# Optimization experiments

Measured on AMD Instinct MI355X. Metric: run time of the kernel, lower is better.

## Reference

```python
import jax, jax.numpy as jnp
import numpy as np

B, IN_DIM, OUT_DIM = 16384, 1024, 512
N_CAPS, CAP_DIM = 8, 16


def squash(x, axis=-1):
    # scale = |x|^2 / (1 + |x|^2) ; out = scale * x / sqrt(|x|^2 + 1e-8)
    sq = jnp.sum(x * x, axis=axis, keepdims=True)
    return (sq / (1.0 + sq)) * x / jnp.sqrt(sq + 1e-8)


def setup_inputs() -> dict:
    key = jax.random.key(0)
    k1, k2, k3, k4 = jax.random.split(key, 4)
    x = jax.random.normal(k1, (B, IN_DIM), dtype=jnp.float32)
    # Linear(in_dim, n_caps*cap_dim) params (kaiming-ish scale)
    Wp = jax.random.normal(k2, (IN_DIM, N_CAPS * CAP_DIM), dtype=jnp.float32) / np.sqrt(IN_DIM)
    bp = jax.random.normal(k3, (N_CAPS * CAP_DIM,), dtype=jnp.float32) * 0.01
    # routing transform W: [n_caps, cap_dim, out_dim], init std 0.02 as in torch code
    W = jax.random.normal(k4, (N_CAPS, CAP_DIM, OUT_DIM), dtype=jnp.float32) * 0.02
    return {"x": x, "Wp": Wp, "bp": bp, "W": W, "n_routing": 3}


def reference(x, Wp, bp, W, n_routing):
    batch = x.shape[0]
    primary = x @ Wp + bp                                   # [B, n*d]
    primary = primary.reshape(batch, N_CAPS, CAP_DIM)       # [B, n, d]
    primary = squash(primary, axis=-1)
    u_hat = jnp.einsum('bnd,ndo->bno', primary, W)          # [B, n, o]
    b = jnp.zeros((batch, N_CAPS, 1), dtype=x.dtype)
    v = None
    for i in range(n_routing):
        c = jax.nn.softmax(b, axis=1)                       # [B, n, 1]
        s = jnp.sum(c * u_hat, axis=1)                      # [B, o]
        v = squash(s, axis=-1)                              # [B, o]
        if i < n_routing - 1:
            agreement = jnp.einsum('bno,bo->bn', u_hat, v)  # [B, n]
            b = b + agreement[..., None]
    return v
```

## Files before the change

kernel.cpp:

```cpp
#include <hip/hip_runtime.h>
#include <hip/hip_bf16.h>
#include <math.h>

typedef __attribute__((ext_vector_type(8))) short bf16x8;
typedef __attribute__((ext_vector_type(8))) unsigned short u16x8;
typedef __attribute__((ext_vector_type(4))) float f32x4;
typedef __attribute__((ext_vector_type(16))) float f32x16;

__device__ __forceinline__ unsigned short f2bf(float f) {
  unsigned u = __float_as_uint(f);
  return (unsigned short)((u + 0x7FFFu + ((u >> 16) & 1u)) >> 16);
}
__device__ __forceinline__ float bf2f(unsigned short h) {
  return __uint_as_float(((unsigned)h) << 16);
}
__device__ __forceinline__ void cvt8pk(const float4& a, const float4& b,
                                       u16x8& h, u16x8& l) {
  float f[8] = {a.x, a.y, a.z, a.w, b.x, b.y, b.z, b.w};
  unsigned* hp = (unsigned*)&h;
  unsigned* lp = (unsigned*)&l;
#pragma unroll
  for (int i = 0; i < 4; ++i) {
    __hip_bfloat162 hb = __float22bfloat162_rn(make_float2(f[2*i], f[2*i+1]));
    unsigned hv = *(unsigned*)&hb;
    hp[i] = hv;
    float r0 = f[2*i]     - __uint_as_float(hv << 16);
    float r1 = f[2*i + 1] - __uint_as_float(hv & 0xFFFF0000u);
    __hip_bfloat162 lb = __float22bfloat162_rn(make_float2(r0, r1));
    lp[i] = *(unsigned*)&lb;
  }
}
__device__ __forceinline__ void cvt8b(const float4& a, const float4& b,
                                      bf16x8& h, bf16x8& l) {
  u16x8 hh, ll;
  cvt8pk(a, b, hh, ll);
  h = *(bf16x8*)&hh;
  l = *(bf16x8*)&ll;
}

#define GLD16(g, l) __builtin_amdgcn_global_load_lds( \
    (const __attribute__((address_space(1))) void*)(g), \
    (__attribute__((address_space(3))) void*)(l), 16, 0, 0)

#define MFMA32(a, b, c) __builtin_amdgcn_mfma_f32_32x32x16_bf16(a, b, c, 0, 0, 0)

__device__ const int PM36[36] = {0,0,0,0,0,0,0,0, 1,1,1,1,1,1,1, 2,2,2,2,2,2,
                                 3,3,3,3,3, 4,4,4,4, 5,5,5, 6,6, 7};
__device__ const int PN36[36] = {0,1,2,3,4,5,6,7, 1,2,3,4,5,6,7, 2,3,4,5,6,7,
                                 3,4,5,6,7, 4,5,6,7, 5,6,7, 6,7, 7};
__device__ __forceinline__ constexpr int gidx(int a, int b) {
  int m = a < b ? a : b, n = a < b ? b : a;
  return m * 8 - (m * (m - 1)) / 2 + (n - m);
}

__global__ __launch_bounds__(256) void caps_prep_all(
    const float* __restrict__ Wp, const float* __restrict__ W,
    unsigned short* __restrict__ th1, unsigned short* __restrict__ tl1,
    unsigned short* __restrict__ th2, unsigned short* __restrict__ tl2,
    float* __restrict__ M)
{
  __shared__ float tile[64][128];
  const int t = threadIdx.x, b = blockIdx.x;
  if (b < 16) {
    const float* src = Wp + (size_t)b * 64 * 128;
#pragma unroll
    for (int i = 0; i < 8; ++i) {
      int j = t + i * 256;
      int kk = j >> 5, q = j & 31;
      *(float4*)&tile[kk][q * 4] = *(const float4*)(src + kk * 128 + q * 4);
    }
    __syncthreads();
    const int col = t >> 1, kg0 = (t & 1) * 4;
    unsigned short hi[32], lo[32];
#pragma unroll
    for (int kk = 0; kk < 32; ++kk) {
      float v = tile[kg0 * 8 + kk][col];
      unsigned short h = f2bf(v);
      hi[kk] = h;
      lo[kk] = f2bf(v - bf2f(h));
    }
#pragma unroll
    for (int i = 0; i < 4; ++i) {
      size_t off = (size_t)b * 8192 + (size_t)(kg0 + i) * 1024 + (size_t)col * 8;
      u16x8 vh, vl;
#pragma unroll
      for (int e = 0; e < 8; ++e) { vh[e] = hi[i * 8 + e]; vl[e] = lo[i * 8 + e]; }
      *(u16x8*)(th1 + off) = vh;
      *(u16x8*)(tl1 + off) = vl;
    }
  } else if (b < 32) {
    int tt = (b - 16) * 256 + t;
#pragma unroll
    for (int h = 0; h < 2; ++h) {
      int c = tt + h * 4096;
      int kt = c >> 12, rem = c & 4095;
      int kg = rem >> 9, col = rem & 511;
      int kbase = kt * 64 + kg * 8;
      u16x8 vh, vl;
#pragma unroll
      for (int e = 0; e < 8; ++e) {
        float v = W[(size_t)(kbase + e) * 512 + col];
        unsigned short hh = f2bf(v);
        vh[e] = hh;
        vl[e] = f2bf(v - bf2f(hh));
      }
      size_t off = ((size_t)(kt * 8 + kg) * 512 + col) * 8;
      *(u16x8*)(th2 + off) = vh;
      *(u16x8*)(tl2 + off) = vl;
    }
  } else {
    int bb = b - 32;
    int a = (bb >> 3) * 16 + (t >> 4);
    int c = (bb & 7) * 16 + (t & 15);
    const float* wa = W + (size_t)a * 512;
    const float* wb = W + (size_t)c * 512;
    float acc = 0.f;
#pragma unroll 4
    for (int o = 0; o < 512; o += 4) {
      float4 xx = *(const float4*)(wa + o);
      float4 yy = *(const float4*)(wb + o);
      acc += xx.x * yy.x + xx.y * yy.y + xx.z * yy.z + xx.w * yy.w;
    }
    M[a * 128 + c] = acc;
  }
}

#define K1BUF 20480

__global__ __launch_bounds__(256) void caps_primary(
    const float* __restrict__ x, const unsigned short* __restrict__ bth,
    const unsigned short* __restrict__ btl, const float* __restrict__ bp,
    float* __restrict__ p_out)
{
  __shared__ unsigned short lds[2 * K1BUF];
  const int tid  = threadIdx.x;
  const int lane = tid & 63;
  const int wn   = tid >> 6;
  const int lc   = lane & 31;
  const int hi   = lane >> 5;
  const int row0 = blockIdx.x * 32;

  const int rowA = tid & 31;
  const int kgA  = tid >> 5;
  const float* xrow = x + (size_t)(row0 + rowA) * 1024 + kgA * 8;

  f32x16 acc;
#pragma unroll
  for (int j = 0; j < 16; ++j) acc[j] = 0.f;

  float4 a0, a1;

#define A_LOAD(kt) do { const float* xp_ = xrow + (kt) * 64; \
    a0 = *(const float4*)(xp_); a1 = *(const float4*)(xp_ + 4); } while (0)

#define B_ISSUE(kt, bufi) do { \
    unsigned short* Bh_ = lds + (bufi) * K1BUF + 4096; \
    unsigned short* Bl_ = lds + (bufi) * K1BUF + 12288; \
    const unsigned short* gh_ = bth + ((size_t)(kt) * 1024 + tid) * 8; \
    const unsigned short* gl_ = btl + ((size_t)(kt) * 1024 + tid) * 8; \
    _Pragma("unroll") for (int c_ = 0; c_ < 4; ++c_) { \
      GLD16(gh_ + c_ * 2048, Bh_ + (c_ * 256 + tid) * 8); \
      GLD16(gl_ + c_ * 2048, Bl_ + (c_ * 256 + tid) * 8); \
    } } while (0)

#define A_WRITE(bufi) do { u16x8 h_, l_; cvt8pk(a0, a1, h_, l_); \
    unsigned short* A_ = lds + (bufi) * K1BUF; \
    *(u16x8*)(A_ + (kgA * 32 + rowA) * 8) = h_; \
    *(u16x8*)(A_ + 2048 + (kgA * 32 + rowA) * 8) = l_; } while (0)

#define COMPUTE(bufi) do { \
    const unsigned short* F = lds + (bufi) * K1BUF; \
    _Pragma("unroll") \
    for (int kk = 0; kk < 4; ++kk) { \
      const int ks = kk * 2 + hi; \
      bf16x8 ah  = *(const bf16x8*)(F + (ks * 32 + lc) * 8); \
      bf16x8 al  = *(const bf16x8*)(F + 2048 + (ks * 32 + lc) * 8); \
      bf16x8 bh  = *(const bf16x8*)(F + 4096  + (ks * 128 + wn * 32 + lc) * 8); \
      bf16x8 blo = *(const bf16x8*)(F + 12288 + (ks * 128 + wn * 32 + lc) * 8); \
      acc = MFMA32(ah, bh,  acc); \
      acc = MFMA32(ah, blo, acc); \
      acc = MFMA32(al, bh,  acc); \
    } } while (0)

  A_LOAD(0);
  B_ISSUE(0, 0);
  A_WRITE(0);
  __syncthreads();

#pragma unroll 2
  for (int kt = 0; kt < 16; ++kt) {
    const int cur = kt & 1;
    if (kt < 15) {
      A_LOAD(kt + 1);
      B_ISSUE(kt + 1, cur ^ 1);
    }
    COMPUTE(cur);
    if (kt < 15) A_WRITE(cur ^ 1);
    __syncthreads();
  }
#undef A_LOAD
#undef B_ISSUE
#undef A_WRITE
#undef COMPUTE

  const int col = wn * 32 + lc;
  const float bpv = bp[col];
#pragma unroll
  for (int r = 0; r < 16; ++r) {
    const int row = (r & 3) + 8 * (r >> 2) + 4 * hi;
    float val = acc[r] + bpv;
    float sq = val * val;
    sq += __shfl_xor(sq, 1); sq += __shfl_xor(sq, 2);
    sq += __shfl_xor(sq, 4); sq += __shfl_xor(sq, 8);
    float sc = (sq / (1.f + sq)) / sqrtf(sq + 1e-8f);
    p_out[(size_t)(row0 + row) * 128 + col] = val * sc;
  }
}

__global__ __launch_bounds__(256, 1) void caps_route_g(
    const float* __restrict__ p_in, const float* __restrict__ Mg,
    float* __restrict__ qout)
{
  __shared__ float p_lds[128 * 66];
  __shared__ float M_lds[16384];
  __shared__ float G_lds[64 * 37];
  __shared__ float cs_lds[64 * 9];
  const int tid  = threadIdx.x;
  const int lane = tid & 63;
  const int w    = tid >> 6;
  const int row0 = blockIdx.x * 64;

#pragma unroll
  for (int i = 0; i < 8; ++i) {
    int j = tid + i * 256;
    int r = j >> 5, c4 = j & 31;
    float4 v = *(const float4*)(p_in + (size_t)(row0 + r) * 128 + c4 * 4);
    p_lds[(c4 * 4 + 0) * 66 + r] = v.x;
    p_lds[(c4 * 4 + 1) * 66 + r] = v.y;
    p_lds[(c4 * 4 + 2) * 66 + r] = v.z;
    p_lds[(c4 * 4 + 3) * 66 + r] = v.w;
  }
#pragma unroll
  for (int i = 0; i < 16; ++i) {
    int j = tid + i * 256;
    *(float4*)&M_lds[j * 4] = *(const float4*)(Mg + j * 4);
  }
  __syncthreads();

  for (int i = 0; i < 9; ++i) {
    const int pi = w * 9 + i;
    const int m = PM36[pi], n = PN36[pi];
    float pm[16], pn[16];
#pragma unroll
    for (int j = 0; j < 16; ++j) pm[j] = p_lds[(m * 16 + j) * 66 + lane];
#pragma unroll
    for (int j = 0; j < 16; ++j) pn[j] = p_lds[(n * 16 + j) * 66 + lane];
    float acc = 0.f;
#pragma unroll
    for (int ii = 0; ii < 16; ++ii) {
      const float* Mr = &M_lds[(n * 16 + ii) * 128 + m * 16];
      float t = 0.f;
#pragma unroll
      for (int j4 = 0; j4 < 4; ++j4) {
        float4 mv = *(const float4*)(Mr + j4 * 4);
        t = fmaf(mv.x, pm[j4 * 4 + 0], t);
        t = fmaf(mv.y, pm[j4 * 4 + 1], t);
        t = fmaf(mv.z, pm[j4 * 4 + 2], t);
        t = fmaf(mv.w, pm[j4 * 4 + 3], t);
      }
      acc = fmaf(pn[ii], t, acc);
    }
    G_lds[lane * 37 + pi] = acc;
  }
  __syncthreads();

  if (w == 0) {
    float Gf[36];
#pragma unroll
    for (int j = 0; j < 36; ++j) Gf[j] = G_lds[lane * 37 + j];
    float bb[8] = {0.f, 0.f, 0.f, 0.f, 0.f, 0.f, 0.f, 0.f};
    float cs[8];
#pragma unroll
    for (int it = 0; it < 3; ++it) {
      float mx = bb[0];
#pragma unroll
      for (int n = 1; n < 8; ++n) mx = fmaxf(mx, bb[n]);
      float e[8], Z = 0.f;
#pragma unroll
      for (int n = 0; n < 8; ++n) { e[n] = expf(bb[n] - mx); Z += e[n]; }
      float inv = 1.f / Z;
      float c[8];
#pragma unroll
      for (int n = 0; n < 8; ++n) c[n] = e[n] * inv;
      float t[8] = {0.f, 0.f, 0.f, 0.f, 0.f, 0.f, 0.f, 0.f};
#pragma unroll
      for (int n = 0; n < 8; ++n)
#pragma unroll
        for (int m2 = 0; m2 < 8; ++m2)
          t[n] = fmaf(Gf[gidx(n, m2)], c[m2], t[n]);
      float ss = 0.f;
#pragma unroll
      for (int n = 0; n < 8; ++n) ss = fmaf(c[n], t[n], ss);
      float scale = (ss / (1.f + ss)) / sqrtf(ss + 1e-8f);
      if (it < 2) {
#pragma unroll
        for (int n = 0; n < 8; ++n) bb[n] += scale * t[n];
      } else {
#pragma unroll
        for (int n = 0; n < 8; ++n) cs[n] = scale * c[n];
      }
    }
#pragma unroll
    for (int n = 0; n < 8; ++n) cs_lds[lane * 9 + n] = cs[n];
  }
  __syncthreads();

#pragma unroll
  for (int i = 0; i < 8; ++i) {
    int j = tid + i * 256;
    int r = j >> 5, c4 = j & 31;
    float4 pv = *(const float4*)(p_in + (size_t)(row0 + r) * 128 + c4 * 4);
    float csv = cs_lds[r * 9 + (c4 >> 2)];
    *(float4*)(qout + (size_t)(row0 + r) * 128 + c4 * 4) =
        make_float4(pv.x * csv, pv.y * csv, pv.z * csv, pv.w * csv);
  }
}

__global__ __launch_bounds__(512) void caps_vout(
    const float* __restrict__ q, const unsigned short* __restrict__ bth,
    const unsigned short* __restrict__ btl, float* __restrict__ out)
{
  __shared__ unsigned short Bsh[32768];
  const int tid  = threadIdx.x;
  const int lane = tid & 63;
  const int w    = tid >> 6;
  const int wm   = w >> 2;
  const int wn   = w & 3;
  const int lc   = lane & 31;
  const int hi   = lane >> 5;
  const int row0 = blockIdx.x * 64;
  const int col0 = blockIdx.y * 128;

#pragma unroll
  for (int i = 0; i < 4; ++i) {
    int idx = tid + i * 512;
    int kt = idx >> 10, kg = (idx >> 7) & 7, col = idx & 127;
    size_t g = ((size_t)(kt * 8 + kg) * 512 + col0 + col) * 8;
    *(u16x8*)&Bsh[idx * 8] = *(const u16x8*)(bth + g);
    *(u16x8*)&Bsh[16384 + idx * 8] = *(const u16x8*)(btl + g);
  }
  __syncthreads();

  const float* qp = q + (size_t)(row0 + wm * 32 + lc) * 128;

  f32x16 acc;
#pragma unroll
  for (int j = 0; j < 16; ++j) acc[j] = 0.f;

#pragma unroll
  for (int kt = 0; kt < 2; ++kt) {
#pragma unroll
    for (int kk = 0; kk < 4; ++kk) {
      const float* qk = qp + kt * 64 + kk * 16 + hi * 8;
      float4 a0 = *(const float4*)(qk);
      float4 a1 = *(const float4*)(qk + 4);
      bf16x8 ah, al;
      cvt8b(a0, a1, ah, al);
      const int ks = kk * 2 + hi;
      const int fi = ((kt * 8 + ks) * 128 + wn * 32 + lc) * 8;
      bf16x8 bh  = *(const bf16x8*)&Bsh[fi];
      bf16x8 blo = *(const bf16x8*)&Bsh[16384 + fi];
      acc = MFMA32(ah, bh,  acc);
      acc = MFMA32(ah, blo, acc);
      acc = MFMA32(al, bh,  acc);
    }
  }

#pragma unroll
  for (int r = 0; r < 16; ++r) {
    const int row = (r & 3) + 8 * (r >> 2) + 4 * hi;
    out[(size_t)(row0 + wm * 32 + row) * 512 + col0 + wn * 32 + lc] = acc[r];
  }
}

extern "C" void kernel_launch(void* const* d_in, const int* in_sizes, int n_in,
                              void* d_out, int out_size, void* d_ws, size_t ws_size,
                              hipStream_t stream) {
  (void)in_sizes; (void)n_in; (void)out_size; (void)ws_size;
  const float* x  = (const float*)d_in[0];
  const float* Wp = (const float*)d_in[1];
  const float* bp = (const float*)d_in[2];
  const float* W  = (const float*)d_in[3];
  char* ws = (char*)d_ws;
  float* p_ws = (float*)ws;
  unsigned short* th1 = (unsigned short*)(ws + 8388608);
  unsigned short* tl1 = (unsigned short*)(ws + 8650752);
  unsigned short* th2 = (unsigned short*)(ws + 8912896);
  unsigned short* tl2 = (unsigned short*)(ws + 9043968);
  float* Mws = (float*)(ws + 9175040);
  float* outp = (float*)d_out;

  caps_prep_all<<<96, 256, 0, stream>>>(Wp, W, th1, tl1, th2, tl2, Mws);
  caps_primary<<<512, 256, 0, stream>>>(x, th1, tl1, bp, p_ws);
  caps_route_g<<<256, 256, 0, stream>>>(p_ws, Mws, p_ws);
  caps_vout<<<dim3(256, 4), 512, 0, stream>>>(p_ws, th2, tl2, outp);
}
```

Measured before the change: 98.78 us.

## Restructure routing Gram kernel to read M from global and shrink LDS footprint

The routing kernel no longer stages the 64KB M matrix in LDS. Each thread now computes one row's full 8-column Gram row (all 64 entries, not the 36 unique ones) with M read through global/cache. Blocks handle 32 rows instead of 64, grid doubles, and the launch-bounds occupancy cap is dropped, so occupancy should rise. The final scaling reuses p from LDS rather than reloading it from global. Separately, the primary GEMM loads x with nontemporal loads. Trade-offs: redundant symmetric Gram work and heavier global/L1 traffic on M.

```diff
diff --git a/kernel.cpp b/kernel.cpp
--- a/kernel.cpp
+++ b/kernel.cpp
@@ -30,6 +30,22 @@
     lp[i] = *(unsigned*)&lb;
   }
 }
+__device__ __forceinline__ void cvt8pk2(const f32x4& a, const f32x4& b,
+                                        u16x8& h, u16x8& l) {
+  float f[8] = {a[0], a[1], a[2], a[3], b[0], b[1], b[2], b[3]};
+  unsigned* hp = (unsigned*)&h;
+  unsigned* lp = (unsigned*)&l;
+#pragma unroll
+  for (int i = 0; i < 4; ++i) {
+    __hip_bfloat162 hb = __float22bfloat162_rn(make_float2(f[2*i], f[2*i+1]));
+    unsigned hv = *(unsigned*)&hb;
+    hp[i] = hv;
+    float r0 = f[2*i]     - __uint_as_float(hv << 16);
+    float r1 = f[2*i + 1] - __uint_as_float(hv & 0xFFFF0000u);
+    __hip_bfloat162 lb = __float22bfloat162_rn(make_float2(r0, r1));
+    lp[i] = *(unsigned*)&lb;
+  }
+}
 __device__ __forceinline__ void cvt8b(const float4& a, const float4& b,
                                       bf16x8& h, bf16x8& l) {
   u16x8 hh, ll;
@@ -43,15 +59,6 @@
     (__attribute__((address_space(3))) void*)(l), 16, 0, 0)
 
 #define MFMA32(a, b, c) __builtin_amdgcn_mfma_f32_32x32x16_bf16(a, b, c, 0, 0, 0)
-
-__device__ const int PM36[36] = {0,0,0,0,0,0,0,0, 1,1,1,1,1,1,1, 2,2,2,2,2,2,
-                                 3,3,3,3,3, 4,4,4,4, 5,5,5, 6,6, 7};
-__device__ const int PN36[36] = {0,1,2,3,4,5,6,7, 1,2,3,4,5,6,7, 2,3,4,5,6,7,
-                                 3,4,5,6,7, 4,5,6,7, 5,6,7, 6,7, 7};
-__device__ __forceinline__ constexpr int gidx(int a, int b) {
-  int m = a < b ? a : b, n = a < b ? b : a;
-  return m * 8 - (m * (m - 1)) / 2 + (n - m);
-}
 
 __global__ __launch_bounds__(256) void caps_prep_all(
     const float* __restrict__ Wp, const float* __restrict__ W,
@@ -148,10 +155,11 @@
 #pragma unroll
   for (int j = 0; j < 16; ++j) acc[j] = 0.f;
 
-  float4 a0, a1;
+  f32x4 a0, a1;
 
 #define A_LOAD(kt) do { const float* xp_ = xrow + (kt) * 64; \
-    a0 = *(const float4*)(xp_); a1 = *(const float4*)(xp_ + 4); } while (0)
+    a0 = __builtin_nontemporal_load((const f32x4*)(xp_)); \
+    a1 = __builtin_nontemporal_load((const f32x4*)(xp_ + 4)); } while (0)
 
 #define B_ISSUE(kt, bufi) do { \
     unsigned short* Bh_ = lds + (bufi) * K1BUF + 4096; \
@@ -163,7 +171,7 @@
       GLD16(gl_ + c_ * 2048, Bl_ + (c_ * 256 + tid) * 8); \
     } } while (0)
 
-#define A_WRITE(bufi) do { u16x8 h_, l_; cvt8pk(a0, a1, h_, l_); \
+#define A_WRITE(bufi) do { u16x8 h_, l_; cvt8pk2(a0, a1, h_, l_); \
     unsigned short* A_ = lds + (bufi) * K1BUF; \
     *(u16x8*)(A_ + (kgA * 32 + rowA) * 8) = h_; \
     *(u16x8*)(A_ + 2048 + (kgA * 32 + rowA) * 8) = l_; } while (0)
@@ -217,67 +225,61 @@
   }
 }
 
-__global__ __launch_bounds__(256, 1) void caps_route_g(
+__global__ __launch_bounds__(256) void caps_route_g(
     const float* __restrict__ p_in, const float* __restrict__ Mg,
     float* __restrict__ qout)
 {
-  __shared__ float p_lds[128 * 66];
-  __shared__ float M_lds[16384];
-  __shared__ float G_lds[64 * 37];
-  __shared__ float cs_lds[64 * 9];
+  __shared__ float p_lds[32 * 132];
+  __shared__ float G_lds[32 * 65];
+  __shared__ float cs_lds[32 * 9];
   const int tid  = threadIdx.x;
-  const int lane = tid & 63;
-  const int w    = tid >> 6;
-  const int row0 = blockIdx.x * 64;
-
-#pragma unroll
-  for (int i = 0; i < 8; ++i) {
+  const int row0 = blockIdx.x * 32;
+
+#pragma unroll
+  for (int i = 0; i < 4; ++i) {
     int j = tid + i * 256;
     int r = j >> 5, c4 = j & 31;
-    float4 v = *(const float4*)(p_in + (size_t)(row0 + r) * 128 + c4 * 4);
-    p_lds[(c4 * 4 + 0) * 66 + r] = v.x;
-    p_lds[(c4 * 4 + 1) * 66 + r] = v.y;
-    p_lds[(c4 * 4 + 2) * 66 + r] = v.z;
-    p_lds[(c4 * 4 + 3) * 66 + r] = v.w;
-  }
-#pragma unroll
-  for (int i = 0; i < 16; ++i) {
-    int j = tid + i * 256;
-    *(float4*)&M_lds[j * 4] = *(const float4*)(Mg + j * 4);
+    *(f32x4*)&p_lds[r * 132 + c4 * 4] =
+        *(const f32x4*)(p_in + (size_t)(row0 + r) * 128 + c4 * 4);
   }
   __syncthreads();
 
-  for (int i = 0; i < 9; ++i) {
-    const int pi = w * 9 + i;
-    const int m = PM36[pi], n = PN36[pi];
-    float pm[16], pn[16];
-#pragma unroll
-    for (int j = 0; j < 16; ++j) pm[j] = p_lds[(m * 16 + j) * 66 + lane];
-#pragma unroll
-    for (int j = 0; j < 16; ++j) pn[j] = p_lds[(n * 16 + j) * 66 + lane];
-    float acc = 0.f;
-#pragma unroll
-    for (int ii = 0; ii < 16; ++ii) {
-      const float* Mr = &M_lds[(n * 16 + ii) * 128 + m * 16];
-      float t = 0.f;
-#pragma unroll
-      for (int j4 = 0; j4 < 4; ++j4) {
-        float4 mv = *(const float4*)(Mr + j4 * 4);
-        t = fmaf(mv.x, pm[j4 * 4 + 0], t);
-        t = fmaf(mv.y, pm[j4 * 4 + 1], t);
-        t = fmaf(mv.z, pm[j4 * 4 + 2], t);
-        t = fmaf(mv.w, pm[j4 * 4 + 3], t);
+  {
+    const int n = tid & 7;
+    const int r = tid >> 3;
+    float pn[16];
+#pragma unroll
+    for (int j = 0; j < 16; ++j) pn[j] = p_lds[r * 132 + n * 16 + j];
+    const float* Mbase = Mg + (size_t)n * 16 * 128;
+#pragma unroll
+    for (int m = 0; m < 8; ++m) {
+      float pm[16];
+#pragma unroll
+      for (int j = 0; j < 16; ++j) pm[j] = p_lds[r * 132 + m * 16 + j];
+      float acc = 0.f;
+#pragma unroll
+      for (int ii = 0; ii < 16; ++ii) {
+        const float* Mr = Mbase + ii * 128 + m * 16;
+        float t = 0.f;
+#pragma unroll
+        for (int j4 = 0; j4 < 4; ++j4) {
+          f32x4 mv = *(const f32x4*)(Mr + j4 * 4);
+          t = fmaf(mv[0], pm[j4 * 4 + 0], t);
+          t = fmaf(mv[1], pm[j4 * 4 + 1], t);
+          t = fmaf(mv[2], pm[j4 * 4 + 2], t);
+          t = fmaf(mv[3], pm[j4 * 4 + 3], t);
+        }
+        acc = fmaf(pn[ii], t, acc);
       }
-      acc = fmaf(pn[ii], t, acc);
-    }
-    G_lds[lane * 37 + pi] = acc;
+      G_lds[r * 65 + n * 8 + m] = acc;
+    }
   }
   __syncthreads();
 
-  if (w == 0) {
-    float Gf[36];
-#pragma unroll
-    for (int j = 0; j < 36; ++j) Gf[j] = G_lds[lane * 37 + j];
+  if (tid < 32) {
+    float Gf[64];
+#pragma unroll
+    for (int j = 0; j < 64; ++j) Gf[j] = G_lds[tid * 65 + j];
     float bb[8] = {0.f, 0.f, 0.f, 0.f, 0.f, 0.f, 0.f, 0.f};
     float cs[8];
 #pragma unroll
@@ -296,8 +298,8 @@
 #pragma unroll
       for (int n = 0; n < 8; ++n)
 #pragma unroll
-        for (int m2 = 0; m2 < 8; ++m2)
-          t[n] = fmaf(Gf[gidx(n, m2)], c[m2], t[n]);
+        for (int m = 0; m < 8; ++m)
+          t[n] = fmaf(Gf[n * 8 + m], c[m], t[n]);
       float ss = 0.f;
 #pragma unroll
       for (int n = 0; n < 8; ++n) ss = fmaf(c[n], t[n], ss);
@@ -311,18 +313,18 @@
       }
     }
 #pragma unroll
-    for (int n = 0; n < 8; ++n) cs_lds[lane * 9 + n] = cs[n];
+    for (int n = 0; n < 8; ++n) cs_lds[tid * 9 + n] = cs[n];
   }
   __syncthreads();
 
 #pragma unroll
-  for (int i = 0; i < 8; ++i) {
+  for (int i = 0; i < 4; ++i) {
     int j = tid + i * 256;
     int r = j >> 5, c4 = j & 31;
-    float4 pv = *(const float4*)(p_in + (size_t)(row0 + r) * 128 + c4 * 4);
+    f32x4 pv = *(const f32x4*)&p_lds[r * 132 + c4 * 4];
     float csv = cs_lds[r * 9 + (c4 >> 2)];
-    *(float4*)(qout + (size_t)(row0 + r) * 128 + c4 * 4) =
-        make_float4(pv.x * csv, pv.y * csv, pv.z * csv, pv.w * csv);
+    f32x4 qv = {pv[0] * csv, pv[1] * csv, pv[2] * csv, pv[3] * csv};
+    *(f32x4*)(qout + (size_t)(row0 + r) * 128 + c4 * 4) = qv;
   }
 }
 
@@ -402,6 +404,6 @@
 
   caps_prep_all<<<96, 256, 0, stream>>>(Wp, W, th1, tl1, th2, tl2, Mws);
   caps_primary<<<512, 256, 0, stream>>>(x, th1, tl1, bp, p_ws);
-  caps_route_g<<<256, 256, 0, stream>>>(p_ws, Mws, p_ws);
+  caps_route_g<<<512, 256, 0, stream>>>(p_ws, Mws, p_ws);
   caps_vout<<<dim3(256, 4), 512, 0, stream>>>(p_ws, th2, tl2, outp);
 }
```

New measurement: 201.2 us. +103.7%, slower.

## Fold routing coefficients into vout GEMM and stream M from global memory

Applied to the files above, without the earlier changes.

The routing kernel now writes only 8 per-row coefficients instead of rewriting the whole scaled primary-capsule matrix, and the output GEMM kernel applies those coefficients to the A operand as it loads it. This removes a full read and write pass over the 8 MB primary buffer. The routing kernel also no longer stages the 64 KB M matrix in LDS; it reads M straight from global/cache with compile-time pair indices, which lowers LDS use and allows more than one block per CU. The trade-off is global/L2 reads of M inside the inner loop and a few extra multiplies in the GEMM loader.

```diff
diff --git a/kernel.cpp b/kernel.cpp
--- a/kernel.cpp
+++ b/kernel.cpp
@@ -44,10 +44,6 @@
 
 #define MFMA32(a, b, c) __builtin_amdgcn_mfma_f32_32x32x16_bf16(a, b, c, 0, 0, 0)
 
-__device__ const int PM36[36] = {0,0,0,0,0,0,0,0, 1,1,1,1,1,1,1, 2,2,2,2,2,2,
-                                 3,3,3,3,3, 4,4,4,4, 5,5,5, 6,6, 7};
-__device__ const int PN36[36] = {0,1,2,3,4,5,6,7, 1,2,3,4,5,6,7, 2,3,4,5,6,7,
-                                 3,4,5,6,7, 4,5,6,7, 5,6,7, 6,7, 7};
 __device__ __forceinline__ constexpr int gidx(int a, int b) {
   int m = a < b ? a : b, n = a < b ? b : a;
   return m * 8 - (m * (m - 1)) / 2 + (n - m);
@@ -217,14 +213,12 @@
   }
 }
 
-__global__ __launch_bounds__(256, 1) void caps_route_g(
+__global__ __launch_bounds__(256) void caps_route_g(
     const float* __restrict__ p_in, const float* __restrict__ Mg,
-    float* __restrict__ qout)
+    float* __restrict__ cs_out)
 {
-  __shared__ float p_lds[128 * 66];
-  __shared__ float M_lds[16384];
-  __shared__ float G_lds[64 * 37];
-  __shared__ float cs_lds[64 * 9];
+  __shared__ float p_lds[128 * 67];
+  __shared__ float G_lds[36 * 65];
   const int tid  = threadIdx.x;
   const int lane = tid & 63;
   const int w    = tid >> 6;
@@ -234,50 +228,52 @@
   for (int i = 0; i < 8; ++i) {
     int j = tid + i * 256;
     int r = j >> 5, c4 = j & 31;
-    float4 v = *(const float4*)(p_in + (size_t)(row0 + r) * 128 + c4 * 4);
-    p_lds[(c4 * 4 + 0) * 66 + r] = v.x;
-    p_lds[(c4 * 4 + 1) * 66 + r] = v.y;
-    p_lds[(c4 * 4 + 2) * 66 + r] = v.z;
-    p_lds[(c4 * 4 + 3) * 66 + r] = v.w;
-  }
-#pragma unroll
-  for (int i = 0; i < 16; ++i) {
-    int j = tid + i * 256;
-    *(float4*)&M_lds[j * 4] = *(const float4*)(Mg + j * 4);
+    f32x4 v = *(const f32x4*)(p_in + (size_t)(row0 + r) * 128 + c4 * 4);
+    p_lds[(c4 * 4 + 0) * 67 + r] = v[0];
+    p_lds[(c4 * 4 + 1) * 67 + r] = v[1];
+    p_lds[(c4 * 4 + 2) * 67 + r] = v[2];
+    p_lds[(c4 * 4 + 3) * 67 + r] = v[3];
   }
   __syncthreads();
 
-  for (int i = 0; i < 9; ++i) {
-    const int pi = w * 9 + i;
-    const int m = PM36[pi], n = PN36[pi];
-    float pm[16], pn[16];
-#pragma unroll
-    for (int j = 0; j < 16; ++j) pm[j] = p_lds[(m * 16 + j) * 66 + lane];
-#pragma unroll
-    for (int j = 0; j < 16; ++j) pn[j] = p_lds[(n * 16 + j) * 66 + lane];
-    float acc = 0.f;
-#pragma unroll
-    for (int ii = 0; ii < 16; ++ii) {
-      const float* Mr = &M_lds[(n * 16 + ii) * 128 + m * 16];
-      float t = 0.f;
-#pragma unroll
-      for (int j4 = 0; j4 < 4; ++j4) {
-        float4 mv = *(const float4*)(Mr + j4 * 4);
-        t = fmaf(mv.x, pm[j4 * 4 + 0], t);
-        t = fmaf(mv.y, pm[j4 * 4 + 1], t);
-        t = fmaf(mv.z, pm[j4 * 4 + 2], t);
-        t = fmaf(mv.w, pm[j4 * 4 + 3], t);
-      }
-      acc = fmaf(pn[ii], t, acc);
-    }
-    G_lds[lane * 37 + pi] = acc;
-  }
+#define DOPAIR(nn, mm) do { \
+    float pn_[16], pm_[16]; \
+    _Pragma("unroll") for (int j = 0; j < 16; ++j) { \
+      pn_[j] = p_lds[((nn) * 16 + j) * 67 + lane]; \
+      pm_[j] = p_lds[((mm) * 16 + j) * 67 + lane]; } \
+    float ta_[16]; \
+    _Pragma("unroll") for (int ii = 0; ii < 16; ++ii) ta_[ii] = 0.f; \
+    _Pragma("unroll") for (int j4 = 0; j4 < 4; ++j4) { \
+      _Pragma("unroll") for (int ii = 0; ii < 16; ++ii) { \
+        f32x4 mv = *(const f32x4*)(Mg + ((nn) * 16 + ii) * 128 + (mm) * 16 + j4 * 4); \
+        ta_[ii] = fmaf(mv[0], pm_[j4 * 4 + 0], ta_[ii]); \
+        ta_[ii] = fmaf(mv[1], pm_[j4 * 4 + 1], ta_[ii]); \
+        ta_[ii] = fmaf(mv[2], pm_[j4 * 4 + 2], ta_[ii]); \
+        ta_[ii] = fmaf(mv[3], pm_[j4 * 4 + 3], ta_[ii]); } } \
+    float g_ = 0.f; \
+    _Pragma("unroll") for (int ii = 0; ii < 16; ++ii) g_ = fmaf(pn_[ii], ta_[ii], g_); \
+    G_lds[gidx(nn, mm) * 65 + lane] = g_; } while (0)
+
+  if (w == 0) {
+    DOPAIR(0,0); DOPAIR(0,1); DOPAIR(0,2); DOPAIR(0,3); DOPAIR(0,4);
+    DOPAIR(0,5); DOPAIR(0,6); DOPAIR(0,7); DOPAIR(1,1);
+  } else if (w == 1) {
+    DOPAIR(1,2); DOPAIR(1,3); DOPAIR(1,4); DOPAIR(1,5); DOPAIR(1,6);
+    DOPAIR(1,7); DOPAIR(2,2); DOPAIR(2,3); DOPAIR(2,4);
+  } else if (w == 2) {
+    DOPAIR(2,5); DOPAIR(2,6); DOPAIR(2,7); DOPAIR(3,3); DOPAIR(3,4);
+    DOPAIR(3,5); DOPAIR(3,6); DOPAIR(3,7); DOPAIR(4,4);
+  } else {
+    DOPAIR(4,5); DOPAIR(4,6); DOPAIR(4,7); DOPAIR(5,5); DOPAIR(5,6);
+    DOPAIR(5,7); DOPAIR(6,6); DOPAIR(6,7); DOPAIR(7,7);
+  }
+#undef DOPAIR
   __syncthreads();
 
   if (w == 0) {
     float Gf[36];
 #pragma unroll
-    for (int j = 0; j < 36; ++j) Gf[j] = G_lds[lane * 37 + j];
+    for (int j = 0; j < 36; ++j) Gf[j] = G_lds[j * 65 + lane];
     float bb[8] = {0.f, 0.f, 0.f, 0.f, 0.f, 0.f, 0.f, 0.f};
     float cs[8];
 #pragma unroll
@@ -296,8 +292,8 @@
 #pragma unroll
       for (int n = 0; n < 8; ++n)
 #pragma unroll
-        for (int m2 = 0; m2 < 8; ++m2)
-          t[n] = fmaf(Gf[gidx(n, m2)], c[m2], t[n]);
+        for (int m = 0; m < 8; ++m)
+          t[n] = fmaf(Gf[gidx(n, m)], c[m], t[n]);
       float ss = 0.f;
 #pragma unroll
       for (int n = 0; n < 8; ++n) ss = fmaf(c[n], t[n], ss);
@@ -310,25 +306,17 @@
         for (int n = 0; n < 8; ++n) cs[n] = scale * c[n];
       }
     }
-#pragma unroll
-    for (int n = 0; n < 8; ++n) cs_lds[lane * 9 + n] = cs[n];
-  }
-  __syncthreads();
-
-#pragma unroll
-  for (int i = 0; i < 8; ++i) {
-    int j = tid + i * 256;
-    int r = j >> 5, c4 = j & 31;
-    float4 pv = *(const float4*)(p_in + (size_t)(row0 + r) * 128 + c4 * 4);
-    float csv = cs_lds[r * 9 + (c4 >> 2)];
-    *(float4*)(qout + (size_t)(row0 + r) * 128 + c4 * 4) =
-        make_float4(pv.x * csv, pv.y * csv, pv.z * csv, pv.w * csv);
+    f32x4 c0 = {cs[0], cs[1], cs[2], cs[3]};
+    f32x4 c1 = {cs[4], cs[5], cs[6], cs[7]};
+    *(f32x4*)(cs_out + (size_t)(row0 + lane) * 8)     = c0;
+    *(f32x4*)(cs_out + (size_t)(row0 + lane) * 8 + 4) = c1;
   }
 }
 
 __global__ __launch_bounds__(512) void caps_vout(
-    const float* __restrict__ q, const unsigned short* __restrict__ bth,
-    const unsigned short* __restrict__ btl, float* __restrict__ out)
+    const float* __restrict__ p, const unsigned short* __restrict__ bth,
+    const unsigned short* __restrict__ btl, const float* __restrict__ cs,
+    float* __restrict__ out)
 {
   __shared__ unsigned short Bsh[32768];
   const int tid  = threadIdx.x;
@@ -349,9 +337,13 @@
     *(u16x8*)&Bsh[idx * 8] = *(const u16x8*)(bth + g);
     *(u16x8*)&Bsh[16384 + idx * 8] = *(const u16x8*)(btl + g);
   }
+
+  const int rA = row0 + wm * 32 + lc;
+  const float* qp = p + (size_t)rA * 128;
+  float cs8[8];
+  *(f32x4*)&cs8[0] = *(const f32x4*)(cs + (size_t)rA * 8);
+  *(f32x4*)&cs8[4] = *(const f32x4*)(cs + (size_t)rA * 8 + 4);
   __syncthreads();
-
-  const float* qp = q + (size_t)(row0 + wm * 32 + lc) * 128;
 
   f32x16 acc;
 #pragma unroll
@@ -364,6 +356,9 @@
       const float* qk = qp + kt * 64 + kk * 16 + hi * 8;
       float4 a0 = *(const float4*)(qk);
       float4 a1 = *(const float4*)(qk + 4);
+      const float cv = cs8[kt * 4 + kk];
+      a0.x *= cv; a0.y *= cv; a0.z *= cv; a0.w *= cv;
+      a1.x *= cv; a1.y *= cv; a1.z *= cv; a1.w *= cv;
       bf16x8 ah, al;
       cvt8b(a0, a1, ah, al);
       const int ks = kk * 2 + hi;
@@ -398,10 +393,11 @@
   unsigned short* th2 = (unsigned short*)(ws + 8912896);
   unsigned short* tl2 = (unsigned short*)(ws + 9043968);
   float* Mws = (float*)(ws + 9175040);
+  float* cs_ws = (float*)(ws + 9240576);
   float* outp = (float*)d_out;
 
   caps_prep_all<<<96, 256, 0, stream>>>(Wp, W, th1, tl1, th2, tl2, Mws);
   caps_primary<<<512, 256, 0, stream>>>(x, th1, tl1, bp, p_ws);
-  caps_route_g<<<256, 256, 0, stream>>>(p_ws, Mws, p_ws);
-  caps_vout<<<dim3(256, 4), 512, 0, stream>>>(p_ws, th2, tl2, outp);
-}
+  caps_route_g<<<256, 256, 0, stream>>>(p_ws, Mws, cs_ws);
+  caps_vout<<<dim3(256, 4), 512, 0, stream>>>(p_ws, th2, tl2, cs_ws, outp);
+}
```

After: 131.2 us. +32.8%, slower.
